# Performance work log

Measured on AMD Instinct MI355X. Metric: run time of the kernel, lower is better.

## Reference

```python
import jax, jax.numpy as jnp
import numpy as np

S, T, U, V = 9, 9, 512, 512   # camera grid and per-view image resolution
H, W, N = 512, 512, 4          # output resolution, number of neighbor cameras
EPS = 1e-6


def setup_inputs() -> dict:
    key = jax.random.key(0)
    k1, k2, k3, k4, k5 = jax.random.split(key, 5)
    data = jax.random.normal(k1, (S, T, U, V, 3), dtype=jnp.float32)
    pixel = jax.random.normal(k2, (H, W), dtype=jnp.float32)
    cam_xyz = jax.random.uniform(k3, (3,), dtype=jnp.float32)
    neighbors = jax.random.randint(k4, (N, 2), 0, S)
    uv = jax.random.randint(k5, (N, H, W, 2), 0, U)
    return {"data": data, "pixel": pixel, "cam_xyz": cam_xyz,
            "neighbors": neighbors, "uv": uv}


def reference(data, pixel, cam_xyz, neighbors, uv):
    h, w = pixel.shape
    n = neighbors.shape[0]
    # bilinear-style weights (rbf=None branch)
    d = cam_xyz[None, :2] - neighbors.astype(cam_xyz.dtype)   # [N,2]
    t = jnp.flip(jnp.abs(d[:, 0] * d[:, 1]), -1)              # [N]
    t = jnp.where(jnp.abs(t) <= EPS, 0.0, t)
    wgt = t / t.sum()
    wgt = jnp.where(jnp.abs(wgt) <= EPS, 0.0, wgt)
    # gather per-neighbor RGB at computed (u,v) for every output pixel
    uf = uv[..., 0].reshape(n, -1)                            # [N,HW]
    vf = uv[..., 1].reshape(n, -1)                            # [N,HW]
    gathered = data[neighbors[:, 0, None], neighbors[:, 1, None], uf, vf]  # [N,HW,3]
    # weighted accumulation, then the same row-major reshape torch does:
    # sum_i (wgt[i]*data[...]).reshape(3,H,W) == (sum_i ...).reshape(3,H,W)
    rgb = jnp.einsum('n,nkc->kc', wgt, gathered).reshape(3, h, w)
    return rgb
```

## Files before the change

### kernel.cpp

```cpp
#include <hip/hip_runtime.h>


#define Td 9
#define Ud 512
#define Vd 512
#define HW (512 * 512)
#define EPSF 1e-6f

__global__ __launch_bounds__(256) void interp_kernel(
    const float* __restrict__ data,
    const float* __restrict__ cam,
    const int* __restrict__ neighbors,
    const int* __restrict__ uv,
    float* __restrict__ out)
{
    const int k = blockIdx.x * blockDim.x + threadIdx.x;
    if (k >= HW) return;

    const float cx = cam[0];
    const float cy = cam[1];
    float t[4];
#pragma unroll
    for (int n = 0; n < 4; ++n) {
        const int ns = neighbors[2 * (3 - n) + 0];
        const int nt = neighbors[2 * (3 - n) + 1];
        const float dx = cx - (float)ns;
        const float dy = cy - (float)nt;
        float v = fabsf(dx * dy);
        t[n] = (v <= EPSF) ? 0.0f : v;
    }
    const float tsum = t[0] + t[1] + t[2] + t[3];

    float acc0 = 0.0f, acc1 = 0.0f, acc2 = 0.0f;
#pragma unroll
    for (int n = 0; n < 4; ++n) {
        float w = t[n] / tsum;
        if (fabsf(w) <= EPSF) w = 0.0f;
        const int ns = neighbors[2 * n + 0];
        const int nt = neighbors[2 * n + 1];
        const int2 uvv = *reinterpret_cast<const int2*>(&uv[((size_t)n * HW + k) * 2]);
        const int off = (((ns * Td + nt) * Ud + uvv.x) * Vd + uvv.y) * 3;
        acc0 += w * data[off + 0];
        acc1 += w * data[off + 1];
        acc2 += w * data[off + 2];
    }

    out[k * 3 + 0] = acc0;
    out[k * 3 + 1] = acc1;
    out[k * 3 + 2] = acc2;
}

extern "C" void kernel_launch(void* const* d_in, const int* in_sizes, int n_in,
                              void* d_out, int out_size, void* d_ws, size_t ws_size,
                              hipStream_t stream)
{
    const float* data      = (const float*)d_in[0];
    const float* cam       = (const float*)d_in[2];
    const int*   neighbors = (const int*)d_in[3];
    const int*   uv        = (const int*)d_in[4];
    float*       out       = (float*)d_out;

    const int threads = 256;
    const int blocks  = (HW + threads - 1) / threads;
    interp_kernel<<<blocks, threads, 0, stream>>>(data, cam, neighbors, uv, out);
}
```

Before: 299.4 us.

## Split gather into per-neighbor-channel partial kernel plus float4 reduction

Each thread now gathers one color channel for one neighbor and writes a weighted partial into workspace. A second kernel sums the four neighbor partials with float4 loads. This exposes more parallelism and memory-level concurrency for the random gathers and makes output writes coalesced. The cost is an extra write and read of a 4x-sized intermediate buffer plus a second launch, and uv is now loaded redundantly by three threads each.

```diff
diff --git a/kernel.cpp b/kernel.cpp
--- a/kernel.cpp
+++ b/kernel.cpp
@@ -4,50 +4,63 @@
 #define Td 9
 #define Ud 512
 #define Vd 512
-#define HW (512 * 512)
+#define HWd (512 * 512)
+#define CH3 (3 * HWd)
 #define EPSF 1e-6f
 
-__global__ __launch_bounds__(256) void interp_kernel(
+__global__ __launch_bounds__(256) void gather_partial(
     const float* __restrict__ data,
     const float* __restrict__ cam,
     const int* __restrict__ neighbors,
     const int* __restrict__ uv,
-    float* __restrict__ out)
+    float* __restrict__ partial)
 {
-    const int k = blockIdx.x * blockDim.x + threadIdx.x;
-    if (k >= HW) return;
+    const int bid  = blockIdx.x;
+    const int slot = bid & 7;
+    const int n    = slot >> 1;
+    const int pb   = ((bid >> 3) << 1) | (slot & 1);
+    const int g    = pb * 256 + threadIdx.x;
+    const int k    = g / 3;
+    const int c    = g - 3 * k;
 
     const float cx = cam[0];
     const float cy = cam[1];
     float t[4];
 #pragma unroll
-    for (int n = 0; n < 4; ++n) {
-        const int ns = neighbors[2 * (3 - n) + 0];
-        const int nt = neighbors[2 * (3 - n) + 1];
-        const float dx = cx - (float)ns;
-        const float dy = cy - (float)nt;
+    for (int m = 0; m < 4; ++m) {
+        const float dx = cx - (float)neighbors[2 * (3 - m) + 0];
+        const float dy = cy - (float)neighbors[2 * (3 - m) + 1];
         float v = fabsf(dx * dy);
-        t[n] = (v <= EPSF) ? 0.0f : v;
+        t[m] = (v <= EPSF) ? 0.0f : v;
     }
     const float tsum = t[0] + t[1] + t[2] + t[3];
+    float w = t[n] / tsum;
+    if (fabsf(w) <= EPSF) w = 0.0f;
 
-    float acc0 = 0.0f, acc1 = 0.0f, acc2 = 0.0f;
-#pragma unroll
-    for (int n = 0; n < 4; ++n) {
-        float w = t[n] / tsum;
-        if (fabsf(w) <= EPSF) w = 0.0f;
-        const int ns = neighbors[2 * n + 0];
-        const int nt = neighbors[2 * n + 1];
-        const int2 uvv = *reinterpret_cast<const int2*>(&uv[((size_t)n * HW + k) * 2]);
-        const int off = (((ns * Td + nt) * Ud + uvv.x) * Vd + uvv.y) * 3;
-        acc0 += w * data[off + 0];
-        acc1 += w * data[off + 1];
-        acc2 += w * data[off + 2];
-    }
+    const int ns = neighbors[2 * n + 0];
+    const int nt = neighbors[2 * n + 1];
+    const int2 uvv = *reinterpret_cast<const int2*>(&uv[((size_t)n * HWd + k) * 2]);
+    const int off = (((ns * Td + nt) * Ud + uvv.x) * Vd + uvv.y) * 3 + c;
 
-    out[k * 3 + 0] = acc0;
-    out[k * 3 + 1] = acc1;
-    out[k * 3 + 2] = acc2;
+    partial[n * CH3 + g] = w * data[off];
+}
+
+__global__ __launch_bounds__(256) void reduce4(
+    const float4* __restrict__ partial,
+    float4* __restrict__ out)
+{
+    const int i = blockIdx.x * blockDim.x + threadIdx.x;
+    const int q = CH3 / 4;
+    float4 a = partial[i];
+    float4 b = partial[q + i];
+    float4 c = partial[2 * q + i];
+    float4 d = partial[3 * q + i];
+    float4 r;
+    r.x = a.x + b.x + c.x + d.x;
+    r.y = a.y + b.y + c.y + d.y;
+    r.z = a.z + b.z + c.z + d.z;
+    r.w = a.w + b.w + c.w + d.w;
+    out[i] = r;
 }
 
 extern "C" void kernel_launch(void* const* d_in, const int* in_sizes, int n_in,
@@ -58,9 +71,10 @@
     const float* cam       = (const float*)d_in[2];
     const int*   neighbors = (const int*)d_in[3];
     const int*   uv        = (const int*)d_in[4];
+    float*       partial   = (float*)d_ws;
     float*       out       = (float*)d_out;
 
-    const int threads = 256;
-    const int blocks  = (HW + threads - 1) / threads;
-    interp_kernel<<<blocks, threads, 0, stream>>>(data, cam, neighbors, uv, out);
+    gather_partial<<<12288, 256, 0, stream>>>(data, cam, neighbors, uv, partial);
+
+    reduce4<<<768, 256, 0, stream>>>((const float4*)partial, (float4*)out);
 }
```

Measured after the change: 304.7 us. Within noise of the previous version (+1.8%).

## Assign one thread per output channel element for coalesced stores and more parallelism

Applied to the files above, without the earlier changes.

Switches from one thread per pixel writing three strided floats to one thread per output element (pixel, channel), so stores are fully coalesced and three times as many threads are in flight to hide gather latency. All four uv loads are hoisted ahead of the gathers to raise memory-level parallelism. In exchange, each uv pair and the weight computation are done three times, and the scattered data gathers become single-float loads repeated across neighbouring threads.

```diff
diff --git a/kernel.cpp b/kernel.cpp
--- a/kernel.cpp
+++ b/kernel.cpp
@@ -4,50 +4,50 @@
 #define Td 9
 #define Ud 512
 #define Vd 512
-#define HW (512 * 512)
+#define HWd (512 * 512)
+#define CH3 (3 * HWd)
 #define EPSF 1e-6f
 
-__global__ __launch_bounds__(256) void interp_kernel(
+__global__ __launch_bounds__(256) void interp_fused(
     const float* __restrict__ data,
     const float* __restrict__ cam,
     const int* __restrict__ neighbors,
     const int* __restrict__ uv,
     float* __restrict__ out)
 {
-    const int k = blockIdx.x * blockDim.x + threadIdx.x;
-    if (k >= HW) return;
+    const unsigned g = blockIdx.x * 256u + threadIdx.x;
+    const unsigned k = g / 3u;
+    const unsigned c = g - 3u * k;
 
     const float cx = cam[0];
     const float cy = cam[1];
     float t[4];
 #pragma unroll
-    for (int n = 0; n < 4; ++n) {
-        const int ns = neighbors[2 * (3 - n) + 0];
-        const int nt = neighbors[2 * (3 - n) + 1];
-        const float dx = cx - (float)ns;
-        const float dy = cy - (float)nt;
+    for (int m = 0; m < 4; ++m) {
+        const float dx = cx - (float)neighbors[2 * (3 - m) + 0];
+        const float dy = cy - (float)neighbors[2 * (3 - m) + 1];
         float v = fabsf(dx * dy);
-        t[n] = (v <= EPSF) ? 0.0f : v;
+        t[m] = (v <= EPSF) ? 0.0f : v;
     }
     const float tsum = t[0] + t[1] + t[2] + t[3];
 
-    float acc0 = 0.0f, acc1 = 0.0f, acc2 = 0.0f;
+    int2 uvv[4];
+#pragma unroll
+    for (int n = 0; n < 4; ++n)
+        uvv[n] = *reinterpret_cast<const int2*>(&uv[((size_t)n * HWd + k) * 2]);
+
+    float acc = 0.0f;
 #pragma unroll
     for (int n = 0; n < 4; ++n) {
         float w = t[n] / tsum;
         if (fabsf(w) <= EPSF) w = 0.0f;
         const int ns = neighbors[2 * n + 0];
         const int nt = neighbors[2 * n + 1];
-        const int2 uvv = *reinterpret_cast<const int2*>(&uv[((size_t)n * HW + k) * 2]);
-        const int off = (((ns * Td + nt) * Ud + uvv.x) * Vd + uvv.y) * 3;
-        acc0 += w * data[off + 0];
-        acc1 += w * data[off + 1];
-        acc2 += w * data[off + 2];
+        const int off = (((ns * Td + nt) * Ud + uvv[n].x) * Vd + uvv[n].y) * 3 + (int)c;
+        acc += w * data[off];
     }
 
-    out[k * 3 + 0] = acc0;
-    out[k * 3 + 1] = acc1;
-    out[k * 3 + 2] = acc2;
+    out[g] = acc;
 }
 
 extern "C" void kernel_launch(void* const* d_in, const int* in_sizes, int n_in,
@@ -60,7 +60,5 @@
     const int*   uv        = (const int*)d_in[4];
     float*       out       = (float*)d_out;
 
-    const int threads = 256;
-    const int blocks  = (HW + threads - 1) / threads;
-    interp_kernel<<<blocks, threads, 0, stream>>>(data, cam, neighbors, uv, out);
+    interp_fused<<<CH3 / 256, 256, 0, stream>>>(data, cam, neighbors, uv, out);
 }
```

Result: no change. 299.7 us (+0.1%).
